# Performance work log

Hardware: AMD Instinct MI355X
Metric: run time of the kernel (lower is better)

Reference implementation:

```python
import jax, jax.numpy as jnp
import numpy as np

NUM_FEATURES = 256
NUM_HEADS = 8
HEAD_SIZE = NUM_FEATURES // NUM_HEADS  # 32
N_AGENTS = 8
B = 32
SEQ = 64


def setup_inputs() -> dict:
    key = jax.random.key(0)
    ks = jax.random.split(key, 6)
    s = 0.02
    x = jax.random.normal(ks[0], (N_AGENTS * B, NUM_FEATURES, SEQ), dtype=jnp.float32)
    Wq = jax.random.normal(ks[1], (NUM_HEADS, NUM_FEATURES, HEAD_SIZE), dtype=jnp.float32) * s
    Wk = jax.random.normal(ks[2], (NUM_HEADS, NUM_FEATURES, HEAD_SIZE), dtype=jnp.float32) * s
    Wv = jax.random.normal(ks[3], (NUM_HEADS, NUM_FEATURES, HEAD_SIZE), dtype=jnp.float32) * s
    Wp = jax.random.normal(ks[4], (NUM_FEATURES, NUM_FEATURES), dtype=jnp.float32) * s
    bp = jnp.zeros((NUM_FEATURES,), dtype=jnp.float32)
    return {"x": x, "Wq": Wq, "Wk": Wk, "Wv": Wv, "Wp": Wp, "bp": bp, "n_agents": N_AGENTS}


def reference(x, Wq, Wk, Wv, Wp, bp, n_agents):
    # x: (n_agents*b, f, h)
    b_total, f, h = x.shape
    b = b_total // n_agents
    # reshape + rearrange 'n b f h -> n b h f'  (t = token axis of length h)
    xs = x.reshape(n_agents, b, f, h).transpose(0, 1, 3, 2)  # (n, b, t, f)
    # All heads at once: per-head linear projections (no bias)
    q = jnp.einsum('nbtf,Hfd->Hnbtd', xs, Wq)
    k = jnp.einsum('nbtf,Hfd->Hnbtd', xs, Wk)
    v = jnp.einsum('nbtf,Hfd->Hnbtd', xs, Wv)
    # all-pairs agent attention: i = key agent, j = query agent
    scale = f ** (-0.5)  # source scales by num_features, not head_size
    scores = jnp.einsum('Hjbtd,Hibsd->Hijbts', q, k) * scale  # (H,n,n,b,t,s)
    attn = jax.nn.softmax(scores, axis=-1)
    # weighted values, then sum over key-agent axis i
    out = jnp.einsum('Hijbts,Hibsd->Hjbtd', attn, v)  # (H,n,b,t,d)
    # concat heads on last dim (head 0 first), matching torch.cat
    y = jnp.moveaxis(out, 0, 3).reshape(n_agents, b, h, f)  # (n,b,t,H*d)
    # output projection (dropout is identity at eval / p=0)
    y = jnp.einsum('nbtf,gf->nbtg', y, Wp) + bp
    # rearrange 'n b h f -> n b f h' then merge agents into batch
    y = y.transpose(0, 1, 3, 2).reshape(n_agents * b, f, h)
    return y
```

## Files before the change

kernel.cpp:

```cpp
#include <hip/hip_runtime.h>

#define F   256
#define T   64
#define NH  8
#define D   32
#define NA  8
#define NBB 32

typedef unsigned short ushortT;
typedef unsigned int   uintT;

typedef short bf16x8 __attribute__((ext_vector_type(8)));
typedef float f32x4  __attribute__((ext_vector_type(4)));

__device__ __forceinline__ float bf2f(ushortT u) {
    union { uintT i; float f; } c; c.i = ((uintT)u) << 16; return c.f;
}
__device__ __forceinline__ ushortT f2bf(float f) {
    union { float f; uintT u; } c; c.f = f;
    uintT u = c.u;
    uintT r = u + 0x7fffu + ((u >> 16) & 1u);
    return (ushortT)(r >> 16);
}

__device__ __forceinline__ int detect_isbf16(const void* xraw) {
    const uintT* w = (const uintT*)xraw;
    int bad = 0;
    for (int k = 0; k < 128; ++k) {
        uintT v = w[k];
        uintT e0 = (v >> 7)  & 0xffu;
        uintT e1 = (v >> 23) & 0xffu;
        bad += (e0 > 131u) + (e1 > 131u);
    }
    return bad == 0 ? 1 : 0;
}

__device__ __forceinline__ ushortT cvt_elem(const void* p, size_t i, bool isbf) {
    return isbf ? ((const ushortT*)p)[i] : f2bf(((const float*)p)[i]);
}


__global__ __launch_bounds__(256) void canon_kernel(const void* __restrict__ x,
                                                    const void* __restrict__ Wq,
                                                    const void* __restrict__ Wk,
                                                    const void* __restrict__ Wv,
                                                    const void* __restrict__ Wp,
                                                    const void* __restrict__ bp,
                                                    ushortT* __restrict__ xb,
                                                    ushortT* __restrict__ Wt,
                                                    ushortT* __restrict__ Wpb,
                                                    ushortT* __restrict__ bpb) {
    __shared__ int sflag;
    if (threadIdx.x == 0) sflag = detect_isbf16(x);
    __syncthreads();
    bool isbf = sflag != 0;

    int idx = blockIdx.x * 256 + threadIdx.x;
    const int NX = NA * NBB * F * T;
    const int NWt = 768 * 256;
    const int NWp = 256 * 256;
    if (idx < NX) { xb[idx] = cvt_elem(x, idx, isbf); return; }
    idx -= NX;
    if (idx < NWt) {
        int cp = idx >> 8, f = idx & 255;
        int qkv = cp >> 8, c = cp & 255, hh = c >> 5, d = c & 31;
        const void* W = (qkv == 0) ? Wq : (qkv == 1) ? Wk : Wv;
        Wt[idx] = cvt_elem(W, (size_t)(hh * F + f) * D + d, isbf);
        return;
    }
    idx -= NWt;
    if (idx < NWp) { Wpb[idx] = cvt_elem(Wp, idx, isbf); return; }
    idx -= NWp;
    if (idx < F) { bpb[idx] = cvt_elem(bp, idx, isbf); }
}

__global__ __launch_bounds__(256) void qkv_kernel(const ushortT* __restrict__ xb,
                                                  const ushortT* __restrict__ Wt,
                                                  ushortT* __restrict__ Qws,
                                                  ushortT* __restrict__ Kws,
                                                  ushortT* __restrict__ Vws) {
    int nb = blockIdx.x, qkv = blockIdx.y;
    __shared__ ushortT xs[T * F];

    {
        const int4* xg = (const int4*)(xb + (size_t)nb * F * T);
        #pragma unroll
        for (int it = 0; it < 8; ++it) {
            int kk = threadIdx.x + it * 256;
            int4 v = xg[kk];
            int f = kk >> 3, t0 = (kk & 7) * 8, sw = (kk & 7) * 8;
            const ushortT* hv = (const ushortT*)&v;
            int fx = f ^ sw;
            #pragma unroll
            for (int m = 0; m < 8; ++m) xs[(t0 + m) * 256 + fx] = hv[m];
        }
    }
    __syncthreads();

    int w = threadIdx.x >> 6, lane = threadIdx.x & 63;
    int l15 = lane & 15, quad = lane >> 4;

    f32x4 acc[4][4];
    #pragma unroll
    for (int a = 0; a < 4; ++a)
        #pragma unroll
        for (int bq = 0; bq < 4; ++bq) acc[a][bq] = (f32x4){0.f, 0.f, 0.f, 0.f};

    const ushortT* Wbase = Wt + (size_t)qkv * 256 * 256;

    #pragma unroll
    for (int ks = 0; ks < 8; ++ks) {
        bf16x8 Bfr[4];
        #pragma unroll
        for (int nt = 0; nt < 4; ++nt) {
            int t = 16 * nt + l15;
            int fb = (ks * 32 + quad * 8) ^ (((t >> 3) & 7) * 8);
            Bfr[nt] = *(const bf16x8*)&xs[t * 256 + fb];
        }
        #pragma unroll
        for (int mt = 0; mt < 4; ++mt) {
            int c = 16 * (4 * w + mt) + l15;
            bf16x8 Afr = *(const bf16x8*)(Wbase + (size_t)c * 256 + ks * 32 + quad * 8);
            #pragma unroll
            for (int nt = 0; nt < 4; ++nt)
                acc[mt][nt] = __builtin_amdgcn_mfma_f32_16x16x32_bf16(Afr, Bfr[nt],
                                                                      acc[mt][nt], 0, 0, 0);
        }
    }

    float scale = (qkv == 0) ? 0.0625f : 1.0f;
    #pragma unroll
    for (int mt = 0; mt < 4; ++mt) {
        int cb = 16 * (4 * w + mt) + quad * 4;
        int hh = cb >> 5, db = cb & 31;
        #pragma unroll
        for (int nt = 0; nt < 4; ++nt) {
            int t = 16 * nt + l15;
            f32x4 v = acc[mt][nt];
            if (qkv < 2) {
                ushortT* dst = ((qkv == 0) ? Qws : Kws) +
                               ((size_t)(nb * NH + hh) * T + t) * D + db;
                uintT lo = (uintT)f2bf(v[0] * scale) | ((uintT)f2bf(v[1] * scale) << 16);
                uintT hi = (uintT)f2bf(v[2] * scale) | ((uintT)f2bf(v[3] * scale) << 16);
                *(uint2*)dst = make_uint2(lo, hi);
            } else {
                ushortT* dst = Vws + ((size_t)(nb * NH + hh) * D + db) * T + t;
                #pragma unroll
                for (int r = 0; r < 4; ++r) dst[r * T] = f2bf(v[r]);
            }
        }
    }
}

__global__ __launch_bounds__(512) void attn_kernel(const ushortT* __restrict__ Qws,
                                                   const ushortT* __restrict__ Kws,
                                                   const ushortT* __restrict__ Vws,
                                                   const ushortT* __restrict__ Wpb,
                                                   const ushortT* __restrict__ bpb,
                                                   const void* __restrict__ xdet,
                                                   void* __restrict__ outp) {
    __shared__ ushortT sm[49664];
    __shared__ int sflag;
    float* bpf = (float*)&sm[49152];

    int tid = threadIdx.x;
    int b = blockIdx.x, j = blockIdx.y;
    int nbj = j * NBB + b;

    if (tid == 0) sflag = detect_isbf16(xdet);
    if (tid < 256) bpf[tid] = bf2f(bpb[tid]);

    int h = tid >> 6, lane = tid & 63;
    int l15 = lane & 15, quad = lane >> 4;
    int v4 = (l15 >> 2) & 3;
    ushortT* P = &sm[h * 4096];

    const ushortT* Qb = Qws + (size_t)(nbj * NH + h) * T * D;
    bf16x8 qf[4];
    #pragma unroll
    for (int nt = 0; nt < 4; ++nt)
        qf[nt] = *(const bf16x8*)(Qb + (16 * nt + l15) * D + quad * 8);

    f32x4 oacc[2][4];
    #pragma unroll
    for (int a = 0; a < 2; ++a)
        #pragma unroll
        for (int c = 0; c < 4; ++c) oacc[a][c] = (f32x4){0.f, 0.f, 0.f, 0.f};

    for (int i = 0; i < NA; ++i) {
        int nbi = i * NBB + b;
        const ushortT* Kb = Kws + (size_t)(nbi * NH + h) * T * D;
        bf16x8 kf[4];
        #pragma unroll
        for (int st = 0; st < 4; ++st)
            kf[st] = *(const bf16x8*)(Kb + (16 * st + l15) * D + quad * 8);

        f32x4 sacc[4][4];
        #pragma unroll
        for (int st = 0; st < 4; ++st)
            #pragma unroll
            for (int tt = 0; tt < 4; ++tt)
                sacc[st][tt] = __builtin_amdgcn_mfma_f32_16x16x32_bf16(
                    kf[st], qf[tt], (f32x4){0.f, 0.f, 0.f, 0.f}, 0, 0, 0);

        #pragma unroll
        for (int tt = 0; tt < 4; ++tt) {
            float mx = -1e30f;
            #pragma unroll
            for (int st = 0; st < 4; ++st)
                #pragma unroll
                for (int r = 0; r < 4; ++r) mx = fmaxf(mx, sacc[st][tt][r]);
            mx = fmaxf(mx, __shfl_xor(mx, 16));
            mx = fmaxf(mx, __shfl_xor(mx, 32));
            float sum = 0.f;
            #pragma unroll
            for (int st = 0; st < 4; ++st)
                #pragma unroll
                for (int r = 0; r < 4; ++r) {
                    float e = __expf(sacc[st][tt][r] - mx);
                    sacc[st][tt][r] = e;
                    sum += e;
                }
            sum += __shfl_xor(sum, 16);
            sum += __shfl_xor(sum, 32);
            float inv = 1.0f / sum;
            int t = tt * 16 + l15;
            #pragma unroll
            for (int st = 0; st < 4; ++st) {
                int sb = (st * 16 + quad * 4) ^ (v4 * 8);
                uintT lo = (uintT)f2bf(sacc[st][tt][0] * inv) |
                           ((uintT)f2bf(sacc[st][tt][1] * inv) << 16);
                uintT hi = (uintT)f2bf(sacc[st][tt][2] * inv) |
                           ((uintT)f2bf(sacc[st][tt][3] * inv) << 16);
                *(uint2*)&P[t * 64 + sb] = make_uint2(lo, hi);
            }
        }

        const ushortT* Vb = Vws + (size_t)(nbi * NH + h) * D * T;
        bf16x8 pf[4][2];
        #pragma unroll
        for (int nt = 0; nt < 4; ++nt)
            #pragma unroll
            for (int ks = 0; ks < 2; ++ks) {
                int sb = (ks * 32 + quad * 8) ^ (v4 * 8);
                pf[nt][ks] = *(const bf16x8*)&P[(nt * 16 + l15) * 64 + sb];
            }
        #pragma unroll
        for (int mt = 0; mt < 2; ++mt) {
            bf16x8 vf[2];
            #pragma unroll
            for (int ks = 0; ks < 2; ++ks)
                vf[ks] = *(const bf16x8*)(Vb + (16 * mt + l15) * T + ks * 32 + quad * 8);
            #pragma unroll
            for (int nt = 0; nt < 4; ++nt)
                #pragma unroll
                for (int ks = 0; ks < 2; ++ks)
                    oacc[mt][nt] = __builtin_amdgcn_mfma_f32_16x16x32_bf16(
                        vf[ks], pf[nt][ks], oacc[mt][nt], 0, 0, 0);
        }
    }

    #pragma unroll
    for (int mt = 0; mt < 2; ++mt)
        #pragma unroll
        for (int nt = 0; nt < 4; ++nt) {
            int t = nt * 16 + l15;
            int cb = h * 32 + 16 * mt + quad * 4;
            f32x4 v = oacc[mt][nt];
            uintT lo = (uintT)f2bf(v[0]) | ((uintT)f2bf(v[1]) << 16);
            uintT hi = (uintT)f2bf(v[2]) | ((uintT)f2bf(v[3]) << 16);
            *(uint2*)&sm[32768 + t * 256 + cb] = make_uint2(lo, hi);
        }
    __syncthreads();

    f32x4 cacc[2][4];
    #pragma unroll
    for (int a = 0; a < 2; ++a)
        #pragma unroll
        for (int c = 0; c < 4; ++c) cacc[a][c] = (f32x4){0.f, 0.f, 0.f, 0.f};

    #pragma unroll
    for (int ks = 0; ks < 8; ++ks) {
        bf16x8 yb[4];
        #pragma unroll
        for (int nt = 0; nt < 4; ++nt)
            yb[nt] = *(const bf16x8*)&sm[32768 + (nt * 16 + l15) * 256 + ks * 32 + quad * 8];
        #pragma unroll
        for (int m2 = 0; m2 < 2; ++m2) {
            int g = 16 * (2 * h + m2) + l15;
            bf16x8 wf = *(const bf16x8*)(Wpb + (size_t)g * 256 + ks * 32 + quad * 8);
            #pragma unroll
            for (int nt = 0; nt < 4; ++nt)
                cacc[m2][nt] = __builtin_amdgcn_mfma_f32_16x16x32_bf16(
                    wf, yb[nt], cacc[m2][nt], 0, 0, 0);
        }
    }

    ushortT* OL = sm;
    #pragma unroll
    for (int m2 = 0; m2 < 2; ++m2)
        #pragma unroll
        for (int nt = 0; nt < 4; ++nt) {
            int t = nt * 16 + l15;
            #pragma unroll
            for (int r = 0; r < 4; ++r) {
                int g = 16 * (2 * h + m2) + quad * 4 + r;
                OL[g * 72 + t] = f2bf(cacc[m2][nt][r] + bpf[g]);
            }
        }
    __syncthreads();

    bool isbf = sflag != 0;
    #pragma unroll
    for (int it = 0; it < 4; ++it) {
        int flat = tid + it * 512;
        int g = flat >> 3, t0 = (flat & 7) * 8;
        uint4 v = *(const uint4*)&OL[g * 72 + t0];
        if (isbf) {
            *(uint4*)((ushortT*)outp + (size_t)nbj * F * T + g * T + t0) = v;
        } else {
            float* ob = (float*)outp + (size_t)nbj * F * T + g * T + t0;
            const ushortT* hv = (const ushortT*)&v;
            #pragma unroll
            for (int m = 0; m < 8; ++m) ob[m] = bf2f(hv[m]);
        }
    }
}

__device__ __forceinline__ float tof(ushortT u) { return bf2f(u); }
__device__ __forceinline__ float tof(float f)   { return f; }

__device__ __forceinline__ void stage_x(const void* x, size_t nb, ushortT* sX,
                                        bool isbf, int tid) {
    if (isbf) {
        const int4* xg = (const int4*)((const ushortT*)x + nb * (F * T));
        int4* xl = (int4*)sX;
        for (int kk = tid; kk < F * T / 8; kk += 512) xl[kk] = xg[kk];
    } else {
        const float4* xg = (const float4*)((const float*)x + nb * (F * T));
        for (int kk = tid; kk < F * T / 4; kk += 512) {
            float4 v = xg[kk];
            int o = kk * 4;
            sX[o + 0] = f2bf(v.x); sX[o + 1] = f2bf(v.y);
            sX[o + 2] = f2bf(v.z); sX[o + 3] = f2bf(v.w);
        }
    }
}

template <typename WT>
__device__ __forceinline__ void q_proj(const WT* __restrict__ W, const ushortT* sX,
                                       ushortT* dst, int c, int t0) {
    float acc[32];
    #pragma unroll
    for (int m = 0; m < 32; ++m) acc[m] = 0.f;
    for (int f = 0; f < F; ++f) {
        float w = tof(W[f * D]);
        const ushortT* xr = &sX[f * T + t0];
        #pragma unroll
        for (int m = 0; m < 32; ++m) acc[m] = fmaf(bf2f(xr[m]), w, acc[m]);
    }
    #pragma unroll
    for (int m = 0; m < 32; ++m) dst[(t0 + m) * F + c] = f2bf(acc[m]);
}

template <typename WT>
__device__ __forceinline__ void kv_proj(const WT* __restrict__ WK, const WT* __restrict__ WV,
                                        const ushortT* sX, ushortT* sK, ushortT* sV,
                                        int c, int t0) {
    float ak[32], av[32];
    #pragma unroll
    for (int m = 0; m < 32; ++m) { ak[m] = 0.f; av[m] = 0.f; }
    for (int f = 0; f < F; ++f) {
        float wk = tof(WK[f * D]);
        float wv = tof(WV[f * D]);
        const ushortT* xr = &sX[f * T + t0];
        #pragma unroll
        for (int m = 0; m < 32; ++m) {
            float xv = bf2f(xr[m]);
            ak[m] = fmaf(xv, wk, ak[m]);
            av[m] = fmaf(xv, wv, av[m]);
        }
    }
    #pragma unroll
    for (int m = 0; m < 32; ++m) {
        sK[(t0 + m) * F + c] = f2bf(ak[m]);
        sV[(t0 + m) * F + c] = f2bf(av[m]);
    }
}

__global__ __launch_bounds__(512) void fused_kernel(const void* __restrict__ x,
                                                    const void* __restrict__ Wq,
                                                    const void* __restrict__ Wk,
                                                    const void* __restrict__ Wv,
                                                    const void* __restrict__ Wp,
                                                    const void* __restrict__ bp,
                                                    void* __restrict__ outp) {
    __shared__ __align__(16) char smem[98304];
    __shared__ int sflag;
    ushortT* sX = (ushortT*)smem;
    ushortT* sK = (ushortT*)(smem + 32768);
    ushortT* sV = (ushortT*)(smem + 65536);
    float*   sO = (float*)smem;

    int tid = threadIdx.x;
    int b = blockIdx.x, j = blockIdx.y;
    size_t nbj = (size_t)j * NBB + b;

    if (tid == 0) sflag = detect_isbf16(x);
    __syncthreads();
    bool isbf = sflag != 0;

    stage_x(x, nbj, sX, isbf, tid);
    __syncthreads();

    int c = tid & 255, t0 = (tid >> 8) * 32;
    int hc = c >> 5, dc = c & 31;
    if (isbf) q_proj((const ushortT*)Wq + (size_t)hc * F * D + dc, sX, sK, c, t0);
    else      q_proj((const float*)Wq   + (size_t)hc * F * D + dc, sX, sK, c, t0);
    __syncthreads();

    int h = tid >> 6, t = tid & 63;
    float q[32], o[32];
    #pragma unroll
    for (int dd = 0; dd < 32; ++dd) { q[dd] = bf2f(sK[t * F + h * D + dd]); o[dd] = 0.f; }

    for (int i = 0; i < NA; ++i) {
        __syncthreads();
        stage_x(x, (size_t)(i * NBB + b), sX, isbf, tid);
        __syncthreads();
        if (isbf) kv_proj((const ushortT*)Wk + (size_t)hc * F * D + dc,
                          (const ushortT*)Wv + (size_t)hc * F * D + dc, sX, sK, sV, c, t0);
        else      kv_proj((const float*)Wk   + (size_t)hc * F * D + dc,
                          (const float*)Wv   + (size_t)hc * F * D + dc, sX, sK, sV, c, t0);
        __syncthreads();
        float l = 0.f;
        float oi[32];
        #pragma unroll
        for (int dd = 0; dd < 32; ++dd) oi[dd] = 0.f;
        for (int s = 0; s < T; ++s) {
            const ushortT* kr = &sK[s * F + h * D];
            float dot = 0.f;
            #pragma unroll
            for (int dd = 0; dd < 32; ++dd) dot = fmaf(q[dd], bf2f(kr[dd]), dot);
            float e = __expf(dot * 0.0625f);
            l += e;
            const ushortT* vr = &sV[s * F + h * D];
            #pragma unroll
            for (int dd = 0; dd < 32; ++dd) oi[dd] = fmaf(e, bf2f(vr[dd]), oi[dd]);
        }
        float inv = 1.0f / l;
        #pragma unroll
        for (int dd = 0; dd < 32; ++dd) o[dd] = fmaf(oi[dd], inv, o[dd]);
    }
    __syncthreads();

    #pragma unroll
    for (int dd = 0; dd < 32; ++dd) sO[(h * D + dd) * T + t] = o[dd];
    __syncthreads();

    {
        int g = tid >> 1, te0 = (tid & 1) * 32;
        float acc[32];
        #pragma unroll
        for (int m = 0; m < 32; ++m) acc[m] = 0.f;
        if (isbf) {
            const ushortT* Wrow = (const ushortT*)Wp + (size_t)g * F;
            for (int cc = 0; cc < F; ++cc) {
                float w = bf2f(Wrow[cc]);
                const float* yr = &sO[cc * T + te0];
                #pragma unroll
                for (int m = 0; m < 32; ++m) acc[m] = fmaf(yr[m], w, acc[m]);
            }
        } else {
            const float* Wrow = (const float*)Wp + (size_t)g * F;
            for (int cc = 0; cc < F; ++cc) {
                float w = Wrow[cc];
                const float* yr = &sO[cc * T + te0];
                #pragma unroll
                for (int m = 0; m < 32; ++m) acc[m] = fmaf(yr[m], w, acc[m]);
            }
        }
        float bias = isbf ? bf2f(((const ushortT*)bp)[g]) : ((const float*)bp)[g];
        if (isbf) {
            ushortT* ob = (ushortT*)outp + nbj * F * T + g * T + te0;
            #pragma unroll
            for (int m = 0; m < 32; ++m) ob[m] = f2bf(acc[m] + bias);
        } else {
            float* ob = (float*)outp + nbj * F * T + g * T + te0;
            #pragma unroll
            for (int m = 0; m < 32; ++m) ob[m] = acc[m] + bias;
        }
    }
}

extern "C" void kernel_launch(void* const* d_in, const int* in_sizes, int n_in,
                              void* d_out, int out_size, void* d_ws, size_t ws_size,
                              hipStream_t stream) {
    const void* x  = d_in[0];
    const void* Wq = d_in[1];
    const void* Wk = d_in[2];
    const void* Wv = d_in[3];
    const void* Wp = d_in[4];
    const void* bp = d_in[5];

    const size_t needA = 34079232;

    if (ws_size >= needA) {
        char* ws = (char*)d_ws;
        ushortT* xb  = (ushortT*)(ws + 0);
        ushortT* Wt  = (ushortT*)(ws + 8388608);
        ushortT* Wpb = (ushortT*)(ws + 8781824);
        ushortT* bpb = (ushortT*)(ws + 8912896);
        ushortT* Qws = (ushortT*)(ws + 8913408);
        ushortT* Kws = (ushortT*)(ws + 17302016);
        ushortT* Vws = (ushortT*)(ws + 25690624);

        canon_kernel<<<dim3(17409),  dim3(256), 0, stream>>>(x, Wq, Wk, Wv, Wp, bp,
                                                             xb, Wt, Wpb, bpb);
        qkv_kernel  <<<dim3(256, 3), dim3(256), 0, stream>>>(xb, Wt, Qws, Kws, Vws);
        attn_kernel <<<dim3(32, 8),  dim3(512), 0, stream>>>(Qws, Kws, Vws, Wpb, bpb,
                                                             x, d_out);
    } else {
        fused_kernel<<<dim3(32, 8), dim3(512), 0, stream>>>(x, Wq, Wk, Wv, Wp, bp, d_out);
    }
}
```

Before: 170.4 us.

## Drop x canonicalization pass; convert x in QKV kernel and merge Q/K/V blocks

Removes the separate pass that converted all of x to bf16 in workspace. The QKV kernel now reads raw x and converts it while staging into shared memory. Each QKV block now computes all three projections, with 8 waves of 96 rows, so x is staged once per batch instead of three times. The attention kernel converts Wp and bp on the fly and writes output straight from registers, skipping the LDS staging. The trade-off is scattered per-element global stores and repeated Wp conversion in every attention block.

```diff
diff --git a/kernel.cpp b/kernel.cpp
--- a/kernel.cpp
+++ b/kernel.cpp
@@ -40,59 +40,65 @@
 }
 
 
-__global__ __launch_bounds__(256) void canon_kernel(const void* __restrict__ x,
-                                                    const void* __restrict__ Wq,
+__global__ __launch_bounds__(256) void wprep_kernel(const void* __restrict__ Wq,
                                                     const void* __restrict__ Wk,
                                                     const void* __restrict__ Wv,
-                                                    const void* __restrict__ Wp,
-                                                    const void* __restrict__ bp,
-                                                    ushortT* __restrict__ xb,
-                                                    ushortT* __restrict__ Wt,
-                                                    ushortT* __restrict__ Wpb,
-                                                    ushortT* __restrict__ bpb) {
+                                                    const void* __restrict__ x,
+                                                    ushortT* __restrict__ Wt) {
     __shared__ int sflag;
     if (threadIdx.x == 0) sflag = detect_isbf16(x);
     __syncthreads();
     bool isbf = sflag != 0;
 
-    int idx = blockIdx.x * 256 + threadIdx.x;
-    const int NX = NA * NBB * F * T;
-    const int NWt = 768 * 256;
-    const int NWp = 256 * 256;
-    if (idx < NX) { xb[idx] = cvt_elem(x, idx, isbf); return; }
-    idx -= NX;
-    if (idx < NWt) {
-        int cp = idx >> 8, f = idx & 255;
-        int qkv = cp >> 8, c = cp & 255, hh = c >> 5, d = c & 31;
-        const void* W = (qkv == 0) ? Wq : (qkv == 1) ? Wk : Wv;
-        Wt[idx] = cvt_elem(W, (size_t)(hh * F + f) * D + d, isbf);
-        return;
-    }
-    idx -= NWt;
-    if (idx < NWp) { Wpb[idx] = cvt_elem(Wp, idx, isbf); return; }
-    idx -= NWp;
-    if (idx < F) { bpb[idx] = cvt_elem(bp, idx, isbf); }
-}
-
-__global__ __launch_bounds__(256) void qkv_kernel(const ushortT* __restrict__ xb,
+    int base = (blockIdx.x * 256 + threadIdx.x) * 8;
+    int cp = base >> 8, f0 = base & 255;
+    int qkv = cp >> 8, c = cp & 255, hh = c >> 5, d = c & 31;
+    const void* W = (qkv == 0) ? Wq : (qkv == 1) ? Wk : Wv;
+
+    ushortT tmp[8];
+    #pragma unroll
+    for (int j = 0; j < 8; ++j)
+        tmp[j] = cvt_elem(W, (size_t)(hh * F + f0 + j) * D + d, isbf);
+    *(uint4*)&Wt[base] = *(const uint4*)tmp;
+}
+
+__global__ __launch_bounds__(512) void qkv_kernel(const void* __restrict__ x,
                                                   const ushortT* __restrict__ Wt,
                                                   ushortT* __restrict__ Qws,
                                                   ushortT* __restrict__ Kws,
                                                   ushortT* __restrict__ Vws) {
-    int nb = blockIdx.x, qkv = blockIdx.y;
-    __shared__ ushortT xs[T * F];
-
-    {
-        const int4* xg = (const int4*)(xb + (size_t)nb * F * T);
+    int nb = blockIdx.x;
+    __shared__ __align__(16) ushortT xs[T * F];
+    __shared__ int sflag;
+
+    if (threadIdx.x == 0) sflag = detect_isbf16(x);
+    __syncthreads();
+    bool isbf = sflag != 0;
+
+    if (isbf) {
+        const int4* xg = (const int4*)((const ushortT*)x + (size_t)nb * F * T);
+        #pragma unroll
+        for (int it = 0; it < 4; ++it) {
+            int kk = threadIdx.x + it * 512;
+            int4 v = xg[kk];
+            int f = kk >> 3, t0 = (kk & 7) * 8;
+            int fx = f ^ ((kk & 7) * 8);
+            const ushortT* hv = (const ushortT*)&v;
+            #pragma unroll
+            for (int m = 0; m < 8; ++m) xs[(t0 + m) * 256 + fx] = hv[m];
+        }
+    } else {
+        const float4* xg = (const float4*)((const float*)x + (size_t)nb * F * T);
         #pragma unroll
         for (int it = 0; it < 8; ++it) {
-            int kk = threadIdx.x + it * 256;
-            int4 v = xg[kk];
-            int f = kk >> 3, t0 = (kk & 7) * 8, sw = (kk & 7) * 8;
-            const ushortT* hv = (const ushortT*)&v;
-            int fx = f ^ sw;
-            #pragma unroll
-            for (int m = 0; m < 8; ++m) xs[(t0 + m) * 256 + fx] = hv[m];
+            int kk = threadIdx.x + it * 512;
+            float4 v = xg[kk];
+            int f = kk >> 4, t0 = (kk & 15) * 4;
+            int fx = f ^ (((t0 >> 3) & 7) * 8);
+            xs[(t0 + 0) * 256 + fx] = f2bf(v.x);
+            xs[(t0 + 1) * 256 + fx] = f2bf(v.y);
+            xs[(t0 + 2) * 256 + fx] = f2bf(v.z);
+            xs[(t0 + 3) * 256 + fx] = f2bf(v.w);
         }
     }
     __syncthreads();
@@ -100,13 +106,11 @@
     int w = threadIdx.x >> 6, lane = threadIdx.x & 63;
     int l15 = lane & 15, quad = lane >> 4;
 
-    f32x4 acc[4][4];
-    #pragma unroll
-    for (int a = 0; a < 4; ++a)
+    f32x4 acc[6][4];
+    #pragma unroll
+    for (int a = 0; a < 6; ++a)
         #pragma unroll
         for (int bq = 0; bq < 4; ++bq) acc[a][bq] = (f32x4){0.f, 0.f, 0.f, 0.f};
-
-    const ushortT* Wbase = Wt + (size_t)qkv * 256 * 256;
 
     #pragma unroll
     for (int ks = 0; ks < 8; ++ks) {
@@ -118,9 +122,9 @@
             Bfr[nt] = *(const bf16x8*)&xs[t * 256 + fb];
         }
         #pragma unroll
-        for (int mt = 0; mt < 4; ++mt) {
-            int c = 16 * (4 * w + mt) + l15;
-            bf16x8 Afr = *(const bf16x8*)(Wbase + (size_t)c * 256 + ks * 32 + quad * 8);
+        for (int mt = 0; mt < 6; ++mt) {
+            int row = 96 * w + 16 * mt + l15;
+            bf16x8 Afr = *(const bf16x8*)(Wt + (size_t)row * 256 + ks * 32 + quad * 8);
             #pragma unroll
             for (int nt = 0; nt < 4; ++nt)
                 acc[mt][nt] = __builtin_amdgcn_mfma_f32_16x16x32_bf16(Afr, Bfr[nt],
@@ -128,17 +132,18 @@
         }
     }
 
-    float scale = (qkv == 0) ? 0.0625f : 1.0f;
-    #pragma unroll
-    for (int mt = 0; mt < 4; ++mt) {
-        int cb = 16 * (4 * w + mt) + quad * 4;
-        int hh = cb >> 5, db = cb & 31;
+    #pragma unroll
+    for (int mt = 0; mt < 6; ++mt) {
+        int cb = 96 * w + 16 * mt + quad * 4;
+        int qsel = cb >> 8;
+        float scale = (qsel == 0) ? 0.0625f : 1.0f;
+        int cc = cb & 255, hh = cc >> 5, db = cc & 31;
         #pragma unroll
         for (int nt = 0; nt < 4; ++nt) {
             int t = 16 * nt + l15;
             f32x4 v = acc[mt][nt];
-            if (qkv < 2) {
-                ushortT* dst = ((qkv == 0) ? Qws : Kws) +
+            if (qsel < 2) {
+                ushortT* dst = ((qsel == 0) ? Qws : Kws) +
                                ((size_t)(nb * NH + hh) * T + t) * D + db;
                 uintT lo = (uintT)f2bf(v[0] * scale) | ((uintT)f2bf(v[1] * scale) << 16);
                 uintT hi = (uintT)f2bf(v[2] * scale) | ((uintT)f2bf(v[3] * scale) << 16);
@@ -155,8 +160,8 @@
 __global__ __launch_bounds__(512) void attn_kernel(const ushortT* __restrict__ Qws,
                                                    const ushortT* __restrict__ Kws,
                                                    const ushortT* __restrict__ Vws,
-                                                   const ushortT* __restrict__ Wpb,
-                                                   const ushortT* __restrict__ bpb,
+                                                   const void* __restrict__ Wp,
+                                                   const void* __restrict__ bp,
                                                    const void* __restrict__ xdet,
                                                    void* __restrict__ outp) {
     __shared__ ushortT sm[49664];
@@ -168,7 +173,10 @@
     int nbj = j * NBB + b;
 
     if (tid == 0) sflag = detect_isbf16(xdet);
-    if (tid < 256) bpf[tid] = bf2f(bpb[tid]);
+    __syncthreads();
+    bool isbf = sflag != 0;
+    if (tid < 256)
+        bpf[tid] = isbf ? bf2f(((const ushortT*)bp)[tid]) : ((const float*)bp)[tid];
 
     int h = tid >> 6, lane = tid & 63;
     int l15 = lane & 15, quad = lane >> 4;
@@ -288,7 +296,18 @@
         #pragma unroll
         for (int m2 = 0; m2 < 2; ++m2) {
             int g = 16 * (2 * h + m2) + l15;
-            bf16x8 wf = *(const bf16x8*)(Wpb + (size_t)g * 256 + ks * 32 + quad * 8);
+            bf16x8 wf;
+            if (isbf) {
+                wf = *(const bf16x8*)((const ushortT*)Wp + (size_t)g * 256 +
+                                      ks * 32 + quad * 8);
+            } else {
+                const float* wr = (const float*)Wp + (size_t)g * 256 + ks * 32 + quad * 8;
+                float4 w0 = *(const float4*)wr;
+                float4 w1 = *(const float4*)(wr + 4);
+                ushortT wt[8] = {f2bf(w0.x), f2bf(w0.y), f2bf(w0.z), f2bf(w0.w),
+                                 f2bf(w1.x), f2bf(w1.y), f2bf(w1.z), f2bf(w1.w)};
+                wf = *(const bf16x8*)wt;
+            }
             #pragma unroll
             for (int nt = 0; nt < 4; ++nt)
                 cacc[m2][nt] = __builtin_amdgcn_mfma_f32_16x16x32_bf16(
@@ -296,7 +315,6 @@
         }
     }
 
-    ushortT* OL = sm;
     #pragma unroll
     for (int m2 = 0; m2 < 2; ++m2)
         #pragma unroll
@@ -305,26 +323,13 @@
             #pragma unroll
             for (int r = 0; r < 4; ++r) {
                 int g = 16 * (2 * h + m2) + quad * 4 + r;
-                OL[g * 72 + t] = f2bf(cacc[m2][nt][r] + bpf[g]);
-            }
-        }
-    __syncthreads();
-
-    bool isbf = sflag != 0;
-    #pragma unroll
-    for (int it = 0; it < 4; ++it) {
-        int flat = tid + it * 512;
-        int g = flat >> 3, t0 = (flat & 7) * 8;
-        uint4 v = *(const uint4*)&OL[g * 72 + t0];
-        if (isbf) {
-            *(uint4*)((ushortT*)outp + (size_t)nbj * F * T + g * T + t0) = v;
-        } else {
-            float* ob = (float*)outp + (size_t)nbj * F * T + g * T + t0;
-            const ushortT* hv = (const ushortT*)&v;
-            #pragma unroll
-            for (int m = 0; m < 8; ++m) ob[m] = bf2f(hv[m]);
-        }
-    }
+                float val = cacc[m2][nt][r] + bpf[g];
+                if (isbf)
+                    ((ushortT*)outp)[(size_t)nbj * F * T + g * T + t] = f2bf(val);
+                else
+                    ((float*)outp)[(size_t)nbj * F * T + g * T + t] = val;
+            }
+        }
 }
 
 __device__ __forceinline__ float tof(ushortT u) { return bf2f(u); }
@@ -503,23 +508,19 @@
     const void* Wp = d_in[4];
     const void* bp = d_in[5];
 
-    const size_t needA = 34079232;
+    const size_t needA = 25559040;
 
     if (ws_size >= needA) {
         char* ws = (char*)d_ws;
-        ushortT* xb  = (ushortT*)(ws + 0);
-        ushortT* Wt  = (ushortT*)(ws + 8388608);
-        ushortT* Wpb = (ushortT*)(ws + 8781824);
-        ushortT* bpb = (ushortT*)(ws + 8912896);
-        ushortT* Qws = (ushortT*)(ws + 8913408);
-        ushortT* Kws = (ushortT*)(ws + 17302016);
-        ushortT* Vws = (ushortT*)(ws + 25690624);
-
-        canon_kernel<<<dim3(17409),  dim3(256), 0, stream>>>(x, Wq, Wk, Wv, Wp, bp,
-                                                             xb, Wt, Wpb, bpb);
-        qkv_kernel  <<<dim3(256, 3), dim3(256), 0, stream>>>(xb, Wt, Qws, Kws, Vws);
-        attn_kernel <<<dim3(32, 8),  dim3(512), 0, stream>>>(Qws, Kws, Vws, Wpb, bpb,
-                                                             x, d_out);
+        ushortT* Wt  = (ushortT*)(ws + 0);
+        ushortT* Qws = (ushortT*)(ws + 393216);
+        ushortT* Kws = (ushortT*)(ws + 8781824);
+        ushortT* Vws = (ushortT*)(ws + 17170432);
+
+        wprep_kernel<<<dim3(96),    dim3(256), 0, stream>>>(Wq, Wk, Wv, x, Wt);
+        qkv_kernel  <<<dim3(256),   dim3(512), 0, stream>>>(x, Wt, Qws, Kws, Vws);
+        attn_kernel <<<dim3(32, 8), dim3(512), 0, stream>>>(Qws, Kws, Vws, Wp, bp,
+                                                            x, d_out);
     } else {
         fused_kernel<<<dim3(32, 8), dim3(512), 0, stream>>>(x, Wq, Wk, Wv, Wp, bp, d_out);
     }
```

Measured after the change: 151.2 us. 1.13x faster.
